# Kernel optimization log

Hardware: AMD Instinct MI355X
Metric: run time of the kernel (lower is better)

Reference implementation:

```python
import jax, jax.numpy as jnp
import numpy as np

BS = 2_000_000
FEAT = 22  # x(3) + R(9) + v(3) + w(3) + u(4)

# Constant physical parameters baked into the module's forward
_M = 1.0 / 0.027                      # inverse mass (Crazyflie, 0.027 kg)
_J = np.diag([2.3951e-05, 2.3951e-05, 3.2347e-05])  # inertia
M1_INV = jnp.asarray(_M * np.eye(3), dtype=jnp.float32)          # M_q_inv1
M2_INV = jnp.asarray(np.linalg.inv(_J), dtype=jnp.float32)       # M_q_inv2
M1 = jnp.asarray(np.linalg.inv(_M * np.eye(3)), dtype=jnp.float32)
M2 = jnp.asarray(_J, dtype=jnp.float32)
MG = jnp.float32(0.027 * 9.81)        # m*g, coefficient of V(q) = m*g*z


def setup_inputs() -> dict:
    key = jax.random.key(0)
    x = jax.random.normal(key, (BS, FEAT), dtype=jnp.float32)
    return {"t": 0, "input": x}


def reference(t, input):
    # split state
    R = input[:, 3:12]
    qdv = input[:, 12:15]   # linear velocity
    qdw = input[:, 15:18]   # angular velocity
    u = input[:, 18:22]     # control

    # momenta: p = M * q_dot  (M = inv(M_q_inv)); matmul(M, v) == v @ M.T
    pv = qdv @ M1.T
    pw = qdw @ M2.T

    # H = pv^T M1inv pv / 2 + pw^T M2inv pw / 2 + m*g*z.
    # H is quadratic in p with SYMMETRIC M_inv and linear in x, so the
    # autograd.grad in the original has the closed form:
    #   dHdpv = M1_inv pv,  dHdpw = M2_inv pw,  dHdx = (0,0,m*g),  dHdR = 0
    dHdpv = pv @ M1_INV.T
    dHdpw = pw @ M2_INV.T

    Rmat = R.reshape(-1, 3, 3)

    dx = jnp.einsum('bij,bj->bi', Rmat, dHdpv)
    dR = jnp.concatenate([
        jnp.cross(Rmat[:, 0, :], dHdpw),
        jnp.cross(Rmat[:, 1, :], dHdpw),
        jnp.cross(Rmat[:, 2, :], dHdpw),
    ], axis=1)

    # F = g_q @ u with g_q = [[0;0],[I4]] row layout -> F = (0, 0, u0, u1, u2, u3)
    Fv = jnp.concatenate([jnp.zeros_like(u[:, :2]), u[:, 0:1]], axis=1)
    Fw = u[:, 1:4]

    # R^T dHdx with dHdx = (0,0,mg) is mg * (third row of R)
    dpv = jnp.cross(pv, dHdpw) - MG * Rmat[:, 2, :] + Fv
    # dHdR = 0 so the cross(R_row, dHdR) terms vanish exactly
    dpw = jnp.cross(pw, dHdpw) + jnp.cross(pv, dHdpv) + Fw

    dv = dpv @ M1_INV.T
    dw = dpw @ M2_INV.T

    return jnp.concatenate([dx, dR, dv, dw, jnp.zeros_like(u)], axis=1)
```

## Files before the change

### kernel.cpp

```cpp
#include <hip/hip_runtime.h>

#define RPB 256

typedef float fvec4 __attribute__((ext_vector_type(4)));

__global__ __launch_bounds__(RPB) void se3_ham_kernel(
    const float* __restrict__ in, float* __restrict__ out, int n_rows) {
    __shared__ float s[RPB * 22];

    const int wave = threadIdx.x >> 6;
    const int lane = threadIdx.x & 63;
    const int row0 = blockIdx.x * RPB + (wave << 6);
    if (row0 >= n_rows) return;
    int count = n_rows - row0;
    if (count > 64) count = 64;
    const int nf  = count * 22;
    const int nf4 = nf >> 2;

    float* const sw = s + wave * (64 * 22);
    fvec4* const s4 = (fvec4*)sw;

    const float* gin  = in + (size_t)row0 * 22;
    const fvec4* gin4 = (const fvec4*)gin;
    for (int i = lane; i < nf4; i += 64)
        s4[i] = __builtin_nontemporal_load(&gin4[i]);
    for (int i = (nf4 << 2) + lane; i < nf; i += 64)
        sw[i] = __builtin_nontemporal_load(&gin[i]);
    __builtin_amdgcn_wave_barrier();

    if (lane < count) {
        float* p = &sw[lane * 22];
        const float R00=p[3],  R01=p[4],  R02=p[5];
        const float R10=p[6],  R11=p[7],  R12=p[8];
        const float R20=p[9],  R21=p[10], R22=p[11];
        const float qv0=p[12], qv1=p[13], qv2=p[14];
        const float qw0=p[15], qw1=p[16], qw2=p[17];
        const float u0 =p[18], u1 =p[19], u2 =p[20], u3=p[21];

        const float M1d   = (float)(1.0 / (1.0 / 0.027));
        const float Minv  = (float)(1.0 / 0.027);
        const float Jx    = (float)2.3951e-05;
        const float Jz    = (float)3.2347e-05;
        const float Jxinv = (float)(1.0 / 2.3951e-05);
        const float Jzinv = (float)(1.0 / 3.2347e-05);
        const float MG    = (float)(0.027 * 9.81);

        const float pv0 = M1d * qv0, pv1 = M1d * qv1, pv2 = M1d * qv2;
        const float pw0 = Jx * qw0,  pw1 = Jx * qw1,  pw2 = Jz * qw2;
        const float hv0 = Minv * pv0, hv1 = Minv * pv1, hv2 = Minv * pv2;
        const float hw0 = Jxinv * pw0, hw1 = Jxinv * pw1, hw2 = Jzinv * pw2;

        const float dpv0 = (pv1*hw2 - pv2*hw1) - MG*R20;
        const float dpv1 = (pv2*hw0 - pv0*hw2) - MG*R21;
        const float dpv2 = (pv0*hw1 - pv1*hw0) - MG*R22 + u0;
        const float dpw0 = (pw1*hw2 - pw2*hw1) + (pv1*hv2 - pv2*hv1) + u1;
        const float dpw1 = (pw2*hw0 - pw0*hw2) + (pv2*hv0 - pv0*hv2) + u2;
        const float dpw2 = (pw0*hw1 - pw1*hw0) + (pv0*hv1 - pv1*hv0) + u3;

        p[0] = R00*hv0 + R01*hv1 + R02*hv2;
        p[1] = R10*hv0 + R11*hv1 + R12*hv2;
        p[2] = R20*hv0 + R21*hv1 + R22*hv2;

        p[3]  = R01*hw2 - R02*hw1;  p[4]  = R02*hw0 - R00*hw2;  p[5]  = R00*hw1 - R01*hw0;
        p[6]  = R11*hw2 - R12*hw1;  p[7]  = R12*hw0 - R10*hw2;  p[8]  = R10*hw1 - R11*hw0;
        p[9]  = R21*hw2 - R22*hw1;  p[10] = R22*hw0 - R20*hw2;  p[11] = R20*hw1 - R21*hw0;

        p[12] = Minv * dpv0;  p[13] = Minv * dpv1;  p[14] = Minv * dpv2;
        p[15] = Jxinv * dpw0; p[16] = Jxinv * dpw1; p[17] = Jzinv * dpw2;

        p[18] = 0.0f; p[19] = 0.0f; p[20] = 0.0f; p[21] = 0.0f;
    }
    __builtin_amdgcn_wave_barrier();

    float* gout  = out + (size_t)row0 * 22;
    fvec4* gout4 = (fvec4*)gout;
    for (int i = lane; i < nf4; i += 64)
        __builtin_nontemporal_store(s4[i], &gout4[i]);
    for (int i = (nf4 << 2) + lane; i < nf; i += 64)
        gout[i] = sw[i];
}

extern "C" void kernel_launch(void* const* d_in, const int* in_sizes, int n_in,
                              void* d_out, int out_size, void* d_ws, size_t ws_size,
                              hipStream_t stream) {
    const float* x = (const float*)d_in[1];
    float* y = (float*)d_out;
    const int n_rows = in_sizes[1] / 22;
    const int blocks = (n_rows + RPB - 1) / RPB;
    se3_ham_kernel<<<blocks, RPB, 0, stream>>>(x, y, n_rows);
}
```

Measured before the change: 288.4 us.

## Replace LDS-staged coalesced copy with direct per-thread vector loads and stores

Drops the shared-memory staging, in which each wave cooperatively copied 64 rows with coalesced 16-byte nontemporal loads and stores. Each thread now reads and writes its own 22-float row directly with memcpy-based 16- and 8-byte accesses. This removes the LDS round trip and the wave barriers. In exchange, global accesses become strided across lanes (88-byte stride), the memcpy calls may be split into narrower accesses because rows are only 8-byte aligned, and the nontemporal hints are lost.

```diff
diff --git a/kernel.cpp b/kernel.cpp
--- a/kernel.cpp
+++ b/kernel.cpp
@@ -1,83 +1,85 @@
 #include <hip/hip_runtime.h>
+#include <stdint.h>
 
-#define RPB 256
-
+typedef float fvec2 __attribute__((ext_vector_type(2)));
 typedef float fvec4 __attribute__((ext_vector_type(4)));
 
-__global__ __launch_bounds__(RPB) void se3_ham_kernel(
+__device__ __forceinline__ fvec4 ld4(const float* p) {
+    fvec4 v; __builtin_memcpy(&v, p, 16); return v;
+}
+__device__ __forceinline__ void st4(float* p, fvec4 v) {
+    __builtin_memcpy(p, &v, 16);
+}
+__device__ __forceinline__ fvec2 ld2(const float* p) {
+    fvec2 v; __builtin_memcpy(&v, p, 8); return v;
+}
+__device__ __forceinline__ void st2(float* p, fvec2 v) {
+    __builtin_memcpy(p, &v, 8);
+}
+
+__global__ __launch_bounds__(256) void se3_ham_kernel(
     const float* __restrict__ in, float* __restrict__ out, int n_rows) {
-    __shared__ float s[RPB * 22];
+    const int row = blockIdx.x * 256 + threadIdx.x;
+    if (row >= n_rows) return;
 
-    const int wave = threadIdx.x >> 6;
-    const int lane = threadIdx.x & 63;
-    const int row0 = blockIdx.x * RPB + (wave << 6);
-    if (row0 >= n_rows) return;
-    int count = n_rows - row0;
-    if (count > 64) count = 64;
-    const int nf  = count * 22;
-    const int nf4 = nf >> 2;
+    const float* p = in + (size_t)row * 22;
+    const fvec4 a0 = ld4(p +  0);
+    const fvec4 a1 = ld4(p +  4);
+    const fvec4 a2 = ld4(p +  8);
+    const fvec4 a3 = ld4(p + 12);
+    const fvec4 a4 = ld4(p + 16);
+    const fvec2 a5 = ld2(p + 20);
 
-    float* const sw = s + wave * (64 * 22);
-    fvec4* const s4 = (fvec4*)sw;
+    const float R00=a0.w, R01=a1.x, R02=a1.y;
+    const float R10=a1.z, R11=a1.w, R12=a2.x;
+    const float R20=a2.y, R21=a2.z, R22=a2.w;
+    const float qv0=a3.x, qv1=a3.y, qv2=a3.z;
+    const float qw0=a3.w, qw1=a4.x, qw2=a4.y;
+    const float u0 =a4.z, u1 =a4.w, u2 =a5.x, u3=a5.y;
 
-    const float* gin  = in + (size_t)row0 * 22;
-    const fvec4* gin4 = (const fvec4*)gin;
-    for (int i = lane; i < nf4; i += 64)
-        s4[i] = __builtin_nontemporal_load(&gin4[i]);
-    for (int i = (nf4 << 2) + lane; i < nf; i += 64)
-        sw[i] = __builtin_nontemporal_load(&gin[i]);
-    __builtin_amdgcn_wave_barrier();
+    const float M1d   = (float)(1.0 / (1.0 / 0.027));
+    const float Minv  = (float)(1.0 / 0.027);
+    const float Jx    = (float)2.3951e-05;
+    const float Jz    = (float)3.2347e-05;
+    const float Jxinv = (float)(1.0 / 2.3951e-05);
+    const float Jzinv = (float)(1.0 / 3.2347e-05);
+    const float MG    = (float)(0.027 * 9.81);
 
-    if (lane < count) {
-        float* p = &sw[lane * 22];
-        const float R00=p[3],  R01=p[4],  R02=p[5];
-        const float R10=p[6],  R11=p[7],  R12=p[8];
-        const float R20=p[9],  R21=p[10], R22=p[11];
-        const float qv0=p[12], qv1=p[13], qv2=p[14];
-        const float qw0=p[15], qw1=p[16], qw2=p[17];
-        const float u0 =p[18], u1 =p[19], u2 =p[20], u3=p[21];
+    const float pv0 = M1d * qv0, pv1 = M1d * qv1, pv2 = M1d * qv2;
+    const float pw0 = Jx * qw0,  pw1 = Jx * qw1,  pw2 = Jz * qw2;
+    const float hv0 = Minv * pv0, hv1 = Minv * pv1, hv2 = Minv * pv2;
+    const float hw0 = Jxinv * pw0, hw1 = Jxinv * pw1, hw2 = Jzinv * pw2;
 
-        const float M1d   = (float)(1.0 / (1.0 / 0.027));
-        const float Minv  = (float)(1.0 / 0.027);
-        const float Jx    = (float)2.3951e-05;
-        const float Jz    = (float)3.2347e-05;
-        const float Jxinv = (float)(1.0 / 2.3951e-05);
-        const float Jzinv = (float)(1.0 / 3.2347e-05);
-        const float MG    = (float)(0.027 * 9.81);
+    const float dpv0 = (pv1*hw2 - pv2*hw1) - MG*R20;
+    const float dpv1 = (pv2*hw0 - pv0*hw2) - MG*R21;
+    const float dpv2 = (pv0*hw1 - pv1*hw0) - MG*R22 + u0;
+    const float dpw0 = (pw1*hw2 - pw2*hw1) + (pv1*hv2 - pv2*hv1) + u1;
+    const float dpw1 = (pw2*hw0 - pw0*hw2) + (pv2*hv0 - pv0*hv2) + u2;
+    const float dpw2 = (pw0*hw1 - pw1*hw0) + (pv0*hv1 - pv1*hv0) + u3;
 
-        const float pv0 = M1d * qv0, pv1 = M1d * qv1, pv2 = M1d * qv2;
-        const float pw0 = Jx * qw0,  pw1 = Jx * qw1,  pw2 = Jz * qw2;
-        const float hv0 = Minv * pv0, hv1 = Minv * pv1, hv2 = Minv * pv2;
-        const float hw0 = Jxinv * pw0, hw1 = Jxinv * pw1, hw2 = Jzinv * pw2;
+    fvec4 r0, r1, r2, r3, r4;
+    fvec2 r5;
+    r0.x = R00*hv0 + R01*hv1 + R02*hv2;
+    r0.y = R10*hv0 + R11*hv1 + R12*hv2;
+    r0.z = R20*hv0 + R21*hv1 + R22*hv2;
+    r0.w = R01*hw2 - R02*hw1;
+    r1.x = R02*hw0 - R00*hw2;  r1.y = R00*hw1 - R01*hw0;
+    r1.z = R11*hw2 - R12*hw1;  r1.w = R12*hw0 - R10*hw2;
+    r2.x = R10*hw1 - R11*hw0;
+    r2.y = R21*hw2 - R22*hw1;  r2.z = R22*hw0 - R20*hw2;  r2.w = R20*hw1 - R21*hw0;
+    r3.x = Minv * dpv0;  r3.y = Minv * dpv1;  r3.z = Minv * dpv2;
+    r3.w = Jxinv * dpw0;
+    r4.x = Jxinv * dpw1; r4.y = Jzinv * dpw2;
+    r4.z = 0.0f; r4.w = 0.0f;
+    r5.x = 0.0f; r5.y = 0.0f;
 
-        const float dpv0 = (pv1*hw2 - pv2*hw1) - MG*R20;
-        const float dpv1 = (pv2*hw0 - pv0*hw2) - MG*R21;
-        const float dpv2 = (pv0*hw1 - pv1*hw0) - MG*R22 + u0;
-        const float dpw0 = (pw1*hw2 - pw2*hw1) + (pv1*hv2 - pv2*hv1) + u1;
-        const float dpw1 = (pw2*hw0 - pw0*hw2) + (pv2*hv0 - pv0*hv2) + u2;
-        const float dpw2 = (pw0*hw1 - pw1*hw0) + (pv0*hv1 - pv1*hv0) + u3;
-
-        p[0] = R00*hv0 + R01*hv1 + R02*hv2;
-        p[1] = R10*hv0 + R11*hv1 + R12*hv2;
-        p[2] = R20*hv0 + R21*hv1 + R22*hv2;
-
-        p[3]  = R01*hw2 - R02*hw1;  p[4]  = R02*hw0 - R00*hw2;  p[5]  = R00*hw1 - R01*hw0;
-        p[6]  = R11*hw2 - R12*hw1;  p[7]  = R12*hw0 - R10*hw2;  p[8]  = R10*hw1 - R11*hw0;
-        p[9]  = R21*hw2 - R22*hw1;  p[10] = R22*hw0 - R20*hw2;  p[11] = R20*hw1 - R21*hw0;
-
-        p[12] = Minv * dpv0;  p[13] = Minv * dpv1;  p[14] = Minv * dpv2;
-        p[15] = Jxinv * dpw0; p[16] = Jxinv * dpw1; p[17] = Jzinv * dpw2;
-
-        p[18] = 0.0f; p[19] = 0.0f; p[20] = 0.0f; p[21] = 0.0f;
-    }
-    __builtin_amdgcn_wave_barrier();
-
-    float* gout  = out + (size_t)row0 * 22;
-    fvec4* gout4 = (fvec4*)gout;
-    for (int i = lane; i < nf4; i += 64)
-        __builtin_nontemporal_store(s4[i], &gout4[i]);
-    for (int i = (nf4 << 2) + lane; i < nf; i += 64)
-        gout[i] = sw[i];
+    float* q = out + (size_t)row * 22;
+    st4(q +  0, r0);
+    st4(q +  4, r1);
+    st4(q +  8, r2);
+    st4(q + 12, r3);
+    st4(q + 16, r4);
+    st2(q + 20, r5);
 }
 
 extern "C" void kernel_launch(void* const* d_in, const int* in_sizes, int n_in,
@@ -86,6 +88,6 @@
     const float* x = (const float*)d_in[1];
     float* y = (float*)d_out;
     const int n_rows = in_sizes[1] / 22;
-    const int blocks = (n_rows + RPB - 1) / RPB;
-    se3_ham_kernel<<<blocks, RPB, 0, stream>>>(x, y, n_rows);
+    const int blocks = (n_rows + 255) / 256;
+    se3_ham_kernel<<<blocks, 256, 0, stream>>>(x, y, n_rows);
 }
```

Result: slower. 307.4 us (+6.6%).
